# Performance work log

Hardware: AMD Instinct MI355X
Metric: run time of the kernel (lower is better)

Reference implementation:

```python
import jax, jax.numpy as jnp
import numpy as np

B, S, E, H = 4, 2048, 512, 8
DH = E // H
EPS = 1e-5

def _ln(x, g, b):
    m = jnp.mean(x, axis=-1, keepdims=True)
    v = jnp.var(x, axis=-1, keepdims=True)
    return (x - m) * jax.lax.rsqrt(v + EPS) * g + b

def setup_inputs() -> dict:
    key = jax.random.key(0)
    ks = jax.random.split(key, 8)
    sc = 0.02
    return {
        "x": jax.random.normal(ks[0], (B, S, E), dtype=jnp.float32),
        "ln1_g": jnp.ones((E,), jnp.float32),
        "ln1_b": jnp.zeros((E,), jnp.float32),
        "in_proj_w": sc * jax.random.normal(ks[1], (3 * E, E), jnp.float32),
        "in_proj_b": jnp.zeros((3 * E,), jnp.float32),
        "out_w": sc * jax.random.normal(ks[2], (E, E), jnp.float32),
        "out_b": jnp.zeros((E,), jnp.float32),
        "ln2_g": jnp.ones((E,), jnp.float32),
        "ln2_b": jnp.zeros((E,), jnp.float32),
        "fc1_w": sc * jax.random.normal(ks[3], (E, E), jnp.float32),
        "fc1_b": jnp.zeros((E,), jnp.float32),
        "fc2_w": sc * jax.random.normal(ks[4], (E, E), jnp.float32),
        "fc2_b": jnp.zeros((E,), jnp.float32),
    }

def reference(x, ln1_g, ln1_b, in_proj_w, in_proj_b, out_w, out_b,
              ln2_g, ln2_b, fc1_w, fc1_b, fc2_w, fc2_b):
    # pre-LN
    z = _ln(x, ln1_g, ln1_b)
    # qkv projection (torch MHA packed in_proj: [3E, E])
    qkv = z @ in_proj_w.T + in_proj_b          # [B,S,3E]
    q, k, v = jnp.split(qkv, 3, axis=-1)
    q = q.reshape(B, S, H, DH)
    k = k.reshape(B, S, H, DH)
    v = v.reshape(B, S, H, DH)
    scores = jnp.einsum("bqhd,bkhd->bhqk", q, k) / np.sqrt(DH).astype(np.float32)
    causal = jnp.triu(jnp.ones((S, S), dtype=bool), k=1)  # True = masked
    neg = jnp.finfo(scores.dtype).min
    scores = jnp.where(causal, neg, scores)
    attn = jax.nn.softmax(scores, axis=-1)      # [B,H,S,S]
    ctx = jnp.einsum("bhqk,bkhd->bqhd", attn, v).reshape(B, S, E)
    attn_out = ctx @ out_w.T + out_b
    # torch MHA with need_weights=True averages over heads by default
    attn_weights = jnp.mean(attn, axis=1)       # [B,S,S]
    z2 = x + attn_out
    y = _ln(z2, ln2_g, ln2_b)
    y = jax.nn.leaky_relu(y @ fc1_w.T + fc1_b, negative_slope=0.01)
    y = y @ fc2_w.T + fc2_b
    y = y + z2
    return (y, attn_weights)
```

## Files before the change

kernel.cpp:

```cpp
#include <hip/hip_runtime.h>

typedef short bf16x8 __attribute__((ext_vector_type(8)));
typedef float f32x4 __attribute__((ext_vector_type(4)));
typedef unsigned short u16x8 __attribute__((ext_vector_type(8)));

#define NB 4
#define SQ 2048
#define EM 512
#define NH 8
#define DHD 64
#define QSCALE 0.1803368801111731f

__device__ __forceinline__ unsigned short f2bf(float x) {
  unsigned u = __float_as_uint(x);
  u += 0x7FFFu + ((u >> 16) & 1u);
  return (unsigned short)(u >> 16);
}

__device__ __forceinline__ int sw8(int row, int col8) { return col8 ^ ((row & 7) << 3); }

__global__ __launch_bounds__(256) void f2bf_kernel(const float* __restrict__ in,
                                                   unsigned short* __restrict__ out, int n) {
  int i = (blockIdx.x * 256 + threadIdx.x) * 8;
  if (i >= n) return;
  f32x4 a = *(const f32x4*)(in + i);
  f32x4 b = *(const f32x4*)(in + i + 4);
  u16x8 o;
#pragma unroll
  for (int j = 0; j < 4; ++j) { o[j] = f2bf(a[j]); o[j + 4] = f2bf(b[j]); }
  *(u16x8*)(out + i) = o;
}

__global__ __launch_bounds__(256) void ln_kernel(const float* __restrict__ x,
                                                 const float* __restrict__ g,
                                                 const float* __restrict__ bb,
                                                 unsigned short* __restrict__ out) {
  int tid = threadIdx.x;
  int row = blockIdx.x * 4 + (tid >> 6);
  int lane = tid & 63;
  size_t base = (size_t)row * EM + lane * 8;
  f32x4 v0 = *(const f32x4*)(x + base);
  f32x4 v1 = *(const f32x4*)(x + base + 4);
  float s = 0.f, q = 0.f;
#pragma unroll
  for (int j = 0; j < 4; ++j) { s += v0[j] + v1[j]; q += v0[j] * v0[j] + v1[j] * v1[j]; }
#pragma unroll
  for (int m = 1; m < 64; m <<= 1) { s += __shfl_xor(s, m); q += __shfl_xor(q, m); }
  float mean = s * (1.f / EM);
  float var = q * (1.f / EM) - mean * mean;
  float rs = rsqrtf(var + 1e-5f);
  f32x4 g0 = *(const f32x4*)(g + lane * 8), g1 = *(const f32x4*)(g + lane * 8 + 4);
  f32x4 b0 = *(const f32x4*)(bb + lane * 8), b1 = *(const f32x4*)(bb + lane * 8 + 4);
  u16x8 o;
#pragma unroll
  for (int j = 0; j < 4; ++j) {
    o[j] = f2bf((v0[j] - mean) * rs * g0[j] + b0[j]);
    o[j + 4] = f2bf((v1[j] - mean) * rs * g1[j] + b1[j]);
  }
  *(u16x8*)(out + base) = o;
}

template <bool LEAKY, bool RESID, bool OUTF32, bool QKV>
__global__ __launch_bounds__(256) void gemm64(
    const unsigned short* __restrict__ A, const unsigned short* __restrict__ Bm,
    const float* __restrict__ bias, const float* __restrict__ resid,
    float* __restrict__ outf, unsigned short* __restrict__ outh,
    unsigned short* __restrict__ qo, unsigned short* __restrict__ ko,
    unsigned short* __restrict__ vo, int M, int N, int K) {
  __shared__ unsigned short As[64][64];
  __shared__ unsigned short Bs[64][64];
  int m0 = blockIdx.x * 64, n0 = blockIdx.y * 64;
  int t = threadIdx.x;
  int ar = t >> 2, ac = (t & 3) * 16;
  int wv = t >> 6, ln = t & 63, lg = ln >> 4, lr = ln & 15;
  f32x4 acc[4];
#pragma unroll
  for (int c = 0; c < 4; ++c)
#pragma unroll
    for (int r = 0; r < 4; ++r) acc[c][r] = 0.f;

  const unsigned short* ag = A + (size_t)(m0 + ar) * K + ac;
  const unsigned short* bg = Bm + (size_t)(n0 + ar) * K + ac;
  for (int k0 = 0; k0 < K; k0 += 64) {
    u16x8 a0 = *(const u16x8*)(ag + k0);
    u16x8 a1 = *(const u16x8*)(ag + k0 + 8);
    u16x8 b0 = *(const u16x8*)(bg + k0);
    u16x8 b1 = *(const u16x8*)(bg + k0 + 8);
    *(u16x8*)&As[ar][sw8(ar, ac)] = a0;
    *(u16x8*)&As[ar][sw8(ar, ac + 8)] = a1;
    *(u16x8*)&Bs[ar][sw8(ar, ac)] = b0;
    *(u16x8*)&Bs[ar][sw8(ar, ac + 8)] = b1;
    __syncthreads();
#pragma unroll
    for (int kk = 0; kk < 64; kk += 32) {
      int arw = wv * 16 + lr;
      bf16x8 af = *(const bf16x8*)&As[arw][sw8(arw, kk + lg * 8)];
#pragma unroll
      for (int c = 0; c < 4; ++c) {
        int brw = c * 16 + lr;
        bf16x8 bf = *(const bf16x8*)&Bs[brw][sw8(brw, kk + lg * 8)];
        acc[c] = __builtin_amdgcn_mfma_f32_16x16x32_bf16(af, bf, acc[c], 0, 0, 0);
      }
    }
    __syncthreads();
  }
#pragma unroll
  for (int c = 0; c < 4; ++c) {
    int C_ = n0 + c * 16 + lr;
    float bv = bias[C_];
#pragma unroll
    for (int r = 0; r < 4; ++r) {
      int R_ = m0 + wv * 16 + lg * 4 + r;
      float v = acc[c][r] + bv;
      if (LEAKY) v = v > 0.f ? v : 0.01f * v;
      if (RESID) v += resid[(size_t)R_ * N + C_];
      if (QKV) {
        int which = C_ >> 9, f = C_ & 511, h = f >> 6, d = f & 63;
        int b_ = R_ >> 11, s_ = R_ & 2047;
        if (which == 0) {
          qo[(((size_t)b_ * NH + h) * SQ + s_) * DHD + d] = f2bf(v * QSCALE);
        } else if (which == 1) {
          ko[(((size_t)b_ * NH + h) * SQ + s_) * DHD + d] = f2bf(v);
        } else {
          vo[(((size_t)b_ * NH + h) * DHD + d) * SQ + s_] = f2bf(v);
        }
      } else if (OUTF32) {
        outf[(size_t)R_ * N + C_] = v;
      } else {
        outh[(size_t)R_ * N + C_] = f2bf(v);
      }
    }
  }
}

__global__ __launch_bounds__(256) void flash_kernel(
    const unsigned short* __restrict__ Q, const unsigned short* __restrict__ Kb,
    const unsigned short* __restrict__ Vt, unsigned short* __restrict__ ctx,
    float* __restrict__ mstat, float* __restrict__ lstat) {
  __shared__ unsigned short Ks[2][64][64];
  __shared__ unsigned short Vs[2][64][64];
  __shared__ unsigned short Ps[4][16][64];
  int h = blockIdx.y, b = blockIdx.z;
  int t = threadIdx.x, wv = t >> 6, ln = t & 63, lg = ln >> 4, lr = ln & 15;
  int ar = t >> 2, ac = (t & 3) * 16;
  size_t headoff = ((size_t)b * NH + h) * SQ;
  const unsigned short* kgb = Kb + (headoff + ar) * DHD + ac;
  const unsigned short* vgb = Vt + (((size_t)b * NH + h) * DHD + ar) * SQ + ac;

  bf16x8 vones;
#pragma unroll
  for (int j = 0; j < 8; ++j) vones[j] = (lr == 0) ? (short)0x3F80 : (short)0;

  for (int half = 0; half < 2; ++half) {
    int qt = half ? blockIdx.x : (31 - blockIdx.x);
    int qb = qt * 64;
    const unsigned short* qrow = Q + (headoff + qb + wv * 16 + lr) * DHD;
    bf16x8 aq0 = *(const bf16x8*)(qrow + lg * 8);
    bf16x8 aq1 = *(const bf16x8*)(qrow + 32 + lg * 8);

    f32x4 cacc[4], lacc;
#pragma unroll
    for (int nd = 0; nd < 4; ++nd)
#pragma unroll
      for (int r = 0; r < 4; ++r) cacc[nd][r] = 0.f;
#pragma unroll
    for (int r = 0; r < 4; ++r) lacc[r] = 0.f;
    float mrun[4];
#pragma unroll
    for (int r = 0; r < 4; ++r) mrun[r] = -__builtin_inff();

    int nkt = qt + 1;
    __syncthreads();
    u16x8 kr0 = *(const u16x8*)(kgb);
    u16x8 kr1 = *(const u16x8*)(kgb + 8);
    u16x8 vr0 = *(const u16x8*)(vgb);
    u16x8 vr1 = *(const u16x8*)(vgb + 8);
    *(u16x8*)&Ks[0][ar][sw8(ar, ac)] = kr0;
    *(u16x8*)&Ks[0][ar][sw8(ar, ac + 8)] = kr1;
    *(u16x8*)&Vs[0][ar][sw8(ar, ac)] = vr0;
    *(u16x8*)&Vs[0][ar][sw8(ar, ac + 8)] = vr1;
    if (nkt > 1) {
      kr0 = *(const u16x8*)(kgb + (size_t)64 * DHD);
      kr1 = *(const u16x8*)(kgb + (size_t)64 * DHD + 8);
      vr0 = *(const u16x8*)(vgb + 64);
      vr1 = *(const u16x8*)(vgb + 64 + 8);
    }

    for (int kt = 0; kt < nkt; ++kt) {
      int cur = kt & 1;
      __syncthreads();
      if (kt + 1 < nkt) {
        int nb = cur ^ 1;
        *(u16x8*)&Ks[nb][ar][sw8(ar, ac)] = kr0;
        *(u16x8*)&Ks[nb][ar][sw8(ar, ac + 8)] = kr1;
        *(u16x8*)&Vs[nb][ar][sw8(ar, ac)] = vr0;
        *(u16x8*)&Vs[nb][ar][sw8(ar, ac + 8)] = vr1;
        if (kt + 2 < nkt) {
          size_t ko2 = (size_t)(kt + 2) * 64;
          kr0 = *(const u16x8*)(kgb + ko2 * DHD);
          kr1 = *(const u16x8*)(kgb + ko2 * DHD + 8);
          vr0 = *(const u16x8*)(vgb + ko2);
          vr1 = *(const u16x8*)(vgb + ko2 + 8);
        }
      }

      float sv[4][4];
      __builtin_amdgcn_s_setprio(1);
#pragma unroll
      for (int nt = 0; nt < 4; ++nt) {
        f32x4 sf;
#pragma unroll
        for (int r = 0; r < 4; ++r) sf[r] = 0.f;
        int brw = nt * 16 + lr;
        bf16x8 bk0 = *(const bf16x8*)&Ks[cur][brw][sw8(brw, lg * 8)];
        bf16x8 bk1 = *(const bf16x8*)&Ks[cur][brw][sw8(brw, 32 + lg * 8)];
        sf = __builtin_amdgcn_mfma_f32_16x16x32_bf16(aq0, bk0, sf, 0, 0, 0);
        sf = __builtin_amdgcn_mfma_f32_16x16x32_bf16(aq1, bk1, sf, 0, 0, 0);
#pragma unroll
        for (int r = 0; r < 4; ++r) sv[nt][r] = sf[r];
      }
      __builtin_amdgcn_s_setprio(0);
      if (kt == nkt - 1) {
        int kbase = kt * 64;
#pragma unroll
        for (int nt = 0; nt < 4; ++nt) {
          int kcol = kbase + nt * 16 + lr;
#pragma unroll
          for (int r = 0; r < 4; ++r) {
            int qr = qb + wv * 16 + lg * 4 + r;
            if (kcol > qr) sv[nt][r] = -__builtin_inff();
          }
        }
      }

      float tmax[4], needmax = 0.f;
#pragma unroll
      for (int r = 0; r < 4; ++r) {
        float tm = fmaxf(fmaxf(sv[0][r], sv[1][r]), fmaxf(sv[2][r], sv[3][r]));
#pragma unroll
        for (int m = 1; m < 16; m <<= 1) tm = fmaxf(tm, __shfl_xor(tm, m));
        tmax[r] = tm;
        needmax = fmaxf(needmax, tm - mrun[r]);
      }
      if (__any(needmax > 8.f)) {
#pragma unroll
        for (int r = 0; r < 4; ++r) {
          float mn = fmaxf(mrun[r], tmax[r]);
          float sc = exp2f(mrun[r] - mn);
          mrun[r] = mn;
          lacc[r] *= sc;
#pragma unroll
          for (int nd = 0; nd < 4; ++nd) cacc[nd][r] *= sc;
        }
      }
#pragma unroll
      for (int r = 0; r < 4; ++r) {
        int prow = lg * 4 + r;
#pragma unroll
        for (int nt = 0; nt < 4; ++nt) {
          float p = exp2f(sv[nt][r] - mrun[r]);
          Ps[wv][prow][sw8(prow, nt * 16 + lr)] = f2bf(p);
        }
      }

      bf16x8 pf0 = *(const bf16x8*)&Ps[wv][lr][sw8(lr, lg * 8)];
      bf16x8 pf1 = *(const bf16x8*)&Ps[wv][lr][sw8(lr, 32 + lg * 8)];
      __builtin_amdgcn_s_setprio(1);
      lacc = __builtin_amdgcn_mfma_f32_16x16x32_bf16(pf0, vones, lacc, 0, 0, 0);
      lacc = __builtin_amdgcn_mfma_f32_16x16x32_bf16(pf1, vones, lacc, 0, 0, 0);
#pragma unroll
      for (int nd = 0; nd < 4; ++nd) {
        int vrw = nd * 16 + lr;
        bf16x8 vf0 = *(const bf16x8*)&Vs[cur][vrw][sw8(vrw, lg * 8)];
        bf16x8 vf1 = *(const bf16x8*)&Vs[cur][vrw][sw8(vrw, 32 + lg * 8)];
        cacc[nd] = __builtin_amdgcn_mfma_f32_16x16x32_bf16(pf0, vf0, cacc[nd], 0, 0, 0);
        cacc[nd] = __builtin_amdgcn_mfma_f32_16x16x32_bf16(pf1, vf1, cacc[nd], 0, 0, 0);
      }
      __builtin_amdgcn_s_setprio(0);
    }

    float inv[4];
#pragma unroll
    for (int r = 0; r < 4; ++r) inv[r] = 1.f / __shfl(lacc[r], ln & 48);
#pragma unroll
    for (int nd = 0; nd < 4; ++nd)
#pragma unroll
      for (int r = 0; r < 4; ++r) {
        size_t dst = ((size_t)b * SQ + qb + wv * 16 + lg * 4 + r) * EM + h * DHD + nd * 16 + lr;
        ctx[dst] = f2bf(cacc[nd][r] * inv[r]);
      }
    if (lr == 0) {
#pragma unroll
      for (int r = 0; r < 4; ++r) {
        int row = qb + wv * 16 + lg * 4 + r;
        mstat[headoff + row] = mrun[r];
        lstat[headoff + row] = 0.125f * inv[r];
      }
    }
  }
}

__global__ __launch_bounds__(256) void attnw_kernel(
    const unsigned short* __restrict__ Q, const unsigned short* __restrict__ Kb,
    const float* __restrict__ mstat, const float* __restrict__ lstat,
    float* __restrict__ aw) {
  int kt = blockIdx.x, qt = blockIdx.y, b = blockIdx.z;
  int qb = qt * 64, kb = kt * 64;
  int t = threadIdx.x;
  float* tile = aw + ((size_t)b * SQ + qb) * SQ + kb;
  if (kt > qt) {
    int row = t >> 2, c = (t & 3) * 16;
    f32x4 z;
#pragma unroll
    for (int j = 0; j < 4; ++j) z[j] = 0.f;
    float* p = tile + (size_t)row * SQ + c;
    *(f32x4*)p = z; *(f32x4*)(p + 4) = z; *(f32x4*)(p + 8) = z; *(f32x4*)(p + 12) = z;
    return;
  }
  __shared__ unsigned short Ks[2][64][64];
  int wv = t >> 6, ln = t & 63, lg = ln >> 4, lr = ln & 15;
  int sr = t >> 2, sc8 = (t & 3) * 16;
  bool diag = (kt == qt);
  size_t khstride = (size_t)SQ * DHD;
  const unsigned short* kg = Kb + (((size_t)b * NH) * SQ + kb + sr) * DHD + sc8;
  const unsigned short* qg = Q + (((size_t)b * NH) * SQ + qb + wv * 16 + lr) * DHD + lg * 8;
  size_t mbase = (size_t)b * NH * SQ + qb + wv * 16 + lg * 4;

  u16x8 ka = *(const u16x8*)kg;
  u16x8 kx = *(const u16x8*)(kg + 8);
  *(u16x8*)&Ks[0][sr][sw8(sr, sc8)] = ka;
  *(u16x8*)&Ks[0][sr][sw8(sr, sc8 + 8)] = kx;
  ka = *(const u16x8*)(kg + khstride);
  kx = *(const u16x8*)(kg + khstride + 8);

  bf16x8 aqc0 = *(const bf16x8*)qg;
  bf16x8 aqc1 = *(const bf16x8*)(qg + 32);
  bf16x8 aqn0 = *(const bf16x8*)(qg + khstride);
  bf16x8 aqn1 = *(const bf16x8*)(qg + khstride + 32);
  float mmc[4], lic[4], mmn[4], lin[4];
#pragma unroll
  for (int r = 0; r < 4; ++r) {
    mmc[r] = mstat[mbase + r];
    lic[r] = lstat[mbase + r];
    mmn[r] = mstat[mbase + SQ + r];
    lin[r] = lstat[mbase + SQ + r];
  }

  f32x4 facc[4];
#pragma unroll
  for (int nt = 0; nt < 4; ++nt)
#pragma unroll
    for (int r = 0; r < 4; ++r) facc[nt][r] = 0.f;

  for (int h = 0; h < NH; ++h) {
    int cur = h & 1;
    __syncthreads();
    if (h + 1 < NH) {
      *(u16x8*)&Ks[cur ^ 1][sr][sw8(sr, sc8)] = ka;
      *(u16x8*)&Ks[cur ^ 1][sr][sw8(sr, sc8 + 8)] = kx;
      if (h + 2 < NH) {
        ka = *(const u16x8*)(kg + (size_t)(h + 2) * khstride);
        kx = *(const u16x8*)(kg + (size_t)(h + 2) * khstride + 8);
      }
    }

#pragma unroll
    for (int nt = 0; nt < 4; ++nt) {
      f32x4 sf;
#pragma unroll
      for (int r = 0; r < 4; ++r) sf[r] = 0.f;
      int brw = nt * 16 + lr;
      bf16x8 bk0 = *(const bf16x8*)&Ks[cur][brw][sw8(brw, lg * 8)];
      bf16x8 bk1 = *(const bf16x8*)&Ks[cur][brw][sw8(brw, 32 + lg * 8)];
      sf = __builtin_amdgcn_mfma_f32_16x16x32_bf16(aqc0, bk0, sf, 0, 0, 0);
      sf = __builtin_amdgcn_mfma_f32_16x16x32_bf16(aqc1, bk1, sf, 0, 0, 0);
#pragma unroll
      for (int r = 0; r < 4; ++r) facc[nt][r] += exp2f(sf[r] - mmc[r]) * lic[r];
    }

    aqc0 = aqn0; aqc1 = aqn1;
#pragma unroll
    for (int r = 0; r < 4; ++r) { mmc[r] = mmn[r]; lic[r] = lin[r]; }
    if (h + 2 < NH) {
      aqn0 = *(const bf16x8*)(qg + (size_t)(h + 2) * khstride);
      aqn1 = *(const bf16x8*)(qg + (size_t)(h + 2) * khstride + 32);
#pragma unroll
      for (int r = 0; r < 4; ++r) {
        mmn[r] = mstat[mbase + (size_t)(h + 2) * SQ + r];
        lin[r] = lstat[mbase + (size_t)(h + 2) * SQ + r];
      }
    }
  }

#pragma unroll
  for (int nt = 0; nt < 4; ++nt) {
    int kc = kb + nt * 16 + lr;
#pragma unroll
    for (int r = 0; r < 4; ++r) {
      int qr = qb + wv * 16 + lg * 4 + r;
      float v = (diag && kc > qr) ? 0.f : facc[nt][r];
      tile[(size_t)(wv * 16 + lg * 4 + r) * SQ + nt * 16 + lr] = v;
    }
  }
}

extern "C" void kernel_launch(void* const* d_in, const int* in_sizes, int n_in,
                              void* d_out, int out_size, void* d_ws, size_t ws_size,
                              hipStream_t stream) {
  (void)in_sizes; (void)n_in; (void)out_size; (void)ws_size;
  const float* x = (const float*)d_in[0];
  const float* ln1g = (const float*)d_in[1];
  const float* ln1b = (const float*)d_in[2];
  const float* wqkv = (const float*)d_in[3];
  const float* bqkv = (const float*)d_in[4];
  const float* wout = (const float*)d_in[5];
  const float* bout = (const float*)d_in[6];
  const float* ln2g = (const float*)d_in[7];
  const float* ln2b = (const float*)d_in[8];
  const float* wfc1 = (const float*)d_in[9];
  const float* bfc1 = (const float*)d_in[10];
  const float* wfc2 = (const float*)d_in[11];
  const float* bfc2 = (const float*)d_in[12];

  char* ws = (char*)d_ws;
  unsigned short* zctx = (unsigned short*)(ws);
  unsigned short* qb_ = (unsigned short*)(ws + 8388608);
  unsigned short* kb_ = (unsigned short*)(ws + 16777216);
  unsigned short* vb_ = (unsigned short*)(ws + 25165824);
  float* z2 = (float*)(ws + 33554432);
  float* mstat = (float*)(ws + 50331648);
  float* lstat = (float*)(ws + 50593792);
  unsigned short* wqkv_h = (unsigned short*)(ws + 50855936);
  unsigned short* wout_h = (unsigned short*)(ws + 52428800);
  unsigned short* wfc1_h = (unsigned short*)(ws + 52953088);
  unsigned short* wfc2_h = (unsigned short*)(ws + 53477376);
  unsigned short* y1 = qb_;
  unsigned short* h1 = kb_;

  float* outy = (float*)d_out;
  float* outw = outy + (size_t)NB * SQ * EM;

  f2bf_kernel<<<384, 256, 0, stream>>>(wqkv, wqkv_h, 786432);
  f2bf_kernel<<<128, 256, 0, stream>>>(wout, wout_h, 262144);
  f2bf_kernel<<<128, 256, 0, stream>>>(wfc1, wfc1_h, 262144);
  f2bf_kernel<<<128, 256, 0, stream>>>(wfc2, wfc2_h, 262144);

  ln_kernel<<<2048, 256, 0, stream>>>(x, ln1g, ln1b, zctx);
  gemm64<false, false, false, true><<<dim3(128, 24), 256, 0, stream>>>(
      zctx, wqkv_h, bqkv, nullptr, nullptr, nullptr, qb_, kb_, vb_, 8192, 1536, 512);
  flash_kernel<<<dim3(16, 8, 4), 256, 0, stream>>>(qb_, kb_, vb_, zctx, mstat, lstat);
  attnw_kernel<<<dim3(32, 32, 4), 256, 0, stream>>>(qb_, kb_, mstat, lstat, outw);
  gemm64<false, true, true, false><<<dim3(128, 8), 256, 0, stream>>>(
      zctx, wout_h, bout, x, z2, nullptr, nullptr, nullptr, nullptr, 8192, 512, 512);
  ln_kernel<<<2048, 256, 0, stream>>>(z2, ln2g, ln2b, y1);
  gemm64<true, false, false, false><<<dim3(128, 8), 256, 0, stream>>>(
      y1, wfc1_h, bfc1, nullptr, nullptr, h1, nullptr, nullptr, nullptr, 8192, 512, 512);
  gemm64<false, true, true, false><<<dim3(128, 8), 256, 0, stream>>>(
      h1, wfc2_h, bfc2, z2, outy, nullptr, nullptr, nullptr, nullptr, 8192, 512, 512);
}
```

Baseline: 204.0 us.

## Use direct global-to-LDS loads with double buffering and lazy row-max reduction

```diff
diff --git a/kernel.cpp b/kernel.cpp
--- a/kernel.cpp
+++ b/kernel.cpp
@@ -18,6 +18,12 @@
 }
 
 __device__ __forceinline__ int sw8(int row, int col8) { return col8 ^ ((row & 7) << 3); }
+
+__device__ __forceinline__ void glds16(const void* g, void* l) {
+  __builtin_amdgcn_global_load_lds(
+      (const __attribute__((address_space(1))) void*)g,
+      (__attribute__((address_space(3))) void*)l, 16, 0, 0);
+}
 
 __global__ __launch_bounds__(256) void f2bf_kernel(const float* __restrict__ in,
                                                    unsigned short* __restrict__ out, int n) {
@@ -67,42 +73,52 @@
     float* __restrict__ outf, unsigned short* __restrict__ outh,
     unsigned short* __restrict__ qo, unsigned short* __restrict__ ko,
     unsigned short* __restrict__ vo, int M, int N, int K) {
-  __shared__ unsigned short As[64][64];
-  __shared__ unsigned short Bs[64][64];
+  __shared__ unsigned short As[2][64][64];
+  __shared__ unsigned short Bs[2][64][64];
   int m0 = blockIdx.x * 64, n0 = blockIdx.y * 64;
   int t = threadIdx.x;
-  int ar = t >> 2, ac = (t & 3) * 16;
   int wv = t >> 6, ln = t & 63, lg = ln >> 4, lr = ln & 15;
+  int rsub = ln >> 3;
+  int csw = ((ln & 7) ^ rsub) * 8;
   f32x4 acc[4];
 #pragma unroll
   for (int c = 0; c < 4; ++c)
 #pragma unroll
     for (int r = 0; r < 4; ++r) acc[c][r] = 0.f;
 
-  const unsigned short* ag = A + (size_t)(m0 + ar) * K + ac;
-  const unsigned short* bg = Bm + (size_t)(n0 + ar) * K + ac;
-  for (int k0 = 0; k0 < K; k0 += 64) {
-    u16x8 a0 = *(const u16x8*)(ag + k0);
-    u16x8 a1 = *(const u16x8*)(ag + k0 + 8);
-    u16x8 b0 = *(const u16x8*)(bg + k0);
-    u16x8 b1 = *(const u16x8*)(bg + k0 + 8);
-    *(u16x8*)&As[ar][sw8(ar, ac)] = a0;
-    *(u16x8*)&As[ar][sw8(ar, ac + 8)] = a1;
-    *(u16x8*)&Bs[ar][sw8(ar, ac)] = b0;
-    *(u16x8*)&Bs[ar][sw8(ar, ac + 8)] = b1;
+  const unsigned short* ag0 = A + (size_t)(m0 + wv * 16 + rsub) * K + csw;
+  const unsigned short* ag1 = A + (size_t)(m0 + wv * 16 + 8 + rsub) * K + csw;
+  const unsigned short* bg0 = Bm + (size_t)(n0 + wv * 16 + rsub) * K + csw;
+  const unsigned short* bg1 = Bm + (size_t)(n0 + wv * 16 + 8 + rsub) * K + csw;
+
+  glds16(ag0, &As[0][wv * 16][0]);
+  glds16(ag1, &As[0][wv * 16 + 8][0]);
+  glds16(bg0, &Bs[0][wv * 16][0]);
+  glds16(bg1, &Bs[0][wv * 16 + 8][0]);
+
+  int nk = K >> 6;
+  for (int ki = 0; ki < nk; ++ki) {
+    int cur = ki & 1;
     __syncthreads();
+    if (ki + 1 < nk) {
+      int nb = cur ^ 1;
+      int ko_ = (ki + 1) * 64;
+      glds16(ag0 + ko_, &As[nb][wv * 16][0]);
+      glds16(ag1 + ko_, &As[nb][wv * 16 + 8][0]);
+      glds16(bg0 + ko_, &Bs[nb][wv * 16][0]);
+      glds16(bg1 + ko_, &Bs[nb][wv * 16 + 8][0]);
+    }
 #pragma unroll
     for (int kk = 0; kk < 64; kk += 32) {
       int arw = wv * 16 + lr;
-      bf16x8 af = *(const bf16x8*)&As[arw][sw8(arw, kk + lg * 8)];
+      bf16x8 af = *(const bf16x8*)&As[cur][arw][sw8(arw, kk + lg * 8)];
 #pragma unroll
       for (int c = 0; c < 4; ++c) {
         int brw = c * 16 + lr;
-        bf16x8 bf = *(const bf16x8*)&Bs[brw][sw8(brw, kk + lg * 8)];
+        bf16x8 bf = *(const bf16x8*)&Bs[cur][brw][sw8(brw, kk + lg * 8)];
         acc[c] = __builtin_amdgcn_mfma_f32_16x16x32_bf16(af, bf, acc[c], 0, 0, 0);
       }
     }
-    __syncthreads();
   }
 #pragma unroll
   for (int c = 0; c < 4; ++c) {
@@ -142,10 +158,13 @@
   __shared__ unsigned short Ps[4][16][64];
   int h = blockIdx.y, b = blockIdx.z;
   int t = threadIdx.x, wv = t >> 6, ln = t & 63, lg = ln >> 4, lr = ln & 15;
-  int ar = t >> 2, ac = (t & 3) * 16;
+  int rsub = ln >> 3;
+  int csw = ((ln & 7) ^ rsub) * 8;
   size_t headoff = ((size_t)b * NH + h) * SQ;
-  const unsigned short* kgb = Kb + (headoff + ar) * DHD + ac;
-  const unsigned short* vgb = Vt + (((size_t)b * NH + h) * DHD + ar) * SQ + ac;
+  const unsigned short* kg0 = Kb + (headoff + wv * 16 + rsub) * DHD + csw;
+  const unsigned short* kg1 = Kb + (headoff + wv * 16 + 8 + rsub) * DHD + csw;
+  const unsigned short* vg0 = Vt + (((size_t)b * NH + h) * DHD + wv * 16 + rsub) * SQ + csw;
+  const unsigned short* vg1 = Vt + (((size_t)b * NH + h) * DHD + wv * 16 + 8 + rsub) * SQ + csw;
 
   bf16x8 vones;
 #pragma unroll
@@ -171,37 +190,21 @@
 
     int nkt = qt + 1;
     __syncthreads();
-    u16x8 kr0 = *(const u16x8*)(kgb);
-    u16x8 kr1 = *(const u16x8*)(kgb + 8);
-    u16x8 vr0 = *(const u16x8*)(vgb);
-    u16x8 vr1 = *(const u16x8*)(vgb + 8);
-    *(u16x8*)&Ks[0][ar][sw8(ar, ac)] = kr0;
-    *(u16x8*)&Ks[0][ar][sw8(ar, ac + 8)] = kr1;
-    *(u16x8*)&Vs[0][ar][sw8(ar, ac)] = vr0;
-    *(u16x8*)&Vs[0][ar][sw8(ar, ac + 8)] = vr1;
-    if (nkt > 1) {
-      kr0 = *(const u16x8*)(kgb + (size_t)64 * DHD);
-      kr1 = *(const u16x8*)(kgb + (size_t)64 * DHD + 8);
-      vr0 = *(const u16x8*)(vgb + 64);
-      vr1 = *(const u16x8*)(vgb + 64 + 8);
-    }
+    glds16(kg0, &Ks[0][wv * 16][0]);
+    glds16(kg1, &Ks[0][wv * 16 + 8][0]);
+    glds16(vg0, &Vs[0][wv * 16][0]);
+    glds16(vg1, &Vs[0][wv * 16 + 8][0]);
 
     for (int kt = 0; kt < nkt; ++kt) {
       int cur = kt & 1;
       __syncthreads();
       if (kt + 1 < nkt) {
         int nb = cur ^ 1;
-        *(u16x8*)&Ks[nb][ar][sw8(ar, ac)] = kr0;
-        *(u16x8*)&Ks[nb][ar][sw8(ar, ac + 8)] = kr1;
-        *(u16x8*)&Vs[nb][ar][sw8(ar, ac)] = vr0;
-        *(u16x8*)&Vs[nb][ar][sw8(ar, ac + 8)] = vr1;
-        if (kt + 2 < nkt) {
-          size_t ko2 = (size_t)(kt + 2) * 64;
-          kr0 = *(const u16x8*)(kgb + ko2 * DHD);
-          kr1 = *(const u16x8*)(kgb + ko2 * DHD + 8);
-          vr0 = *(const u16x8*)(vgb + ko2);
-          vr1 = *(const u16x8*)(vgb + ko2 + 8);
-        }
+        size_t ko_ = (size_t)(kt + 1) * 64;
+        glds16(kg0 + ko_ * DHD, &Ks[nb][wv * 16][0]);
+        glds16(kg1 + ko_ * DHD, &Ks[nb][wv * 16 + 8][0]);
+        glds16(vg0 + ko_, &Vs[nb][wv * 16][0]);
+        glds16(vg1 + ko_, &Vs[nb][wv * 16 + 8][0]);
       }
 
       float sv[4][4];
@@ -233,19 +236,20 @@
         }
       }
 
-      float tmax[4], needmax = 0.f;
+      float lmax[4];
+      bool need = false;
 #pragma unroll
       for (int r = 0; r < 4; ++r) {
-        float tm = fmaxf(fmaxf(sv[0][r], sv[1][r]), fmaxf(sv[2][r], sv[3][r]));
-#pragma unroll
-        for (int m = 1; m < 16; m <<= 1) tm = fmaxf(tm, __shfl_xor(tm, m));
-        tmax[r] = tm;
-        needmax = fmaxf(needmax, tm - mrun[r]);
-      }
-      if (__any(needmax > 8.f)) {
+        lmax[r] = fmaxf(fmaxf(sv[0][r], sv[1][r]), fmaxf(sv[2][r], sv[3][r]));
+        need |= (lmax[r] > mrun[r] + 8.f);
+      }
+      if (__any(need)) {
 #pragma unroll
         for (int r = 0; r < 4; ++r) {
-          float mn = fmaxf(mrun[r], tmax[r]);
+          float tm = lmax[r];
+#pragma unroll
+          for (int m = 1; m < 16; m <<= 1) tm = fmaxf(tm, __shfl_xor(tm, m));
+          float mn = fmaxf(mrun[r], tm);
           float sc = exp2f(mrun[r] - mn);
           mrun[r] = mn;
           lacc[r] *= sc;
@@ -319,19 +323,17 @@
   }
   __shared__ unsigned short Ks[2][64][64];
   int wv = t >> 6, ln = t & 63, lg = ln >> 4, lr = ln & 15;
-  int sr = t >> 2, sc8 = (t & 3) * 16;
+  int rsub = ln >> 3;
+  int csw = ((ln & 7) ^ rsub) * 8;
   bool diag = (kt == qt);
   size_t khstride = (size_t)SQ * DHD;
-  const unsigned short* kg = Kb + (((size_t)b * NH) * SQ + kb + sr) * DHD + sc8;
+  const unsigned short* kg0 = Kb + (((size_t)b * NH) * SQ + kb + wv * 16 + rsub) * DHD + csw;
+  const unsigned short* kg1 = Kb + (((size_t)b * NH) * SQ + kb + wv * 16 + 8 + rsub) * DHD + csw;
   const unsigned short* qg = Q + (((size_t)b * NH) * SQ + qb + wv * 16 + lr) * DHD + lg * 8;
   size_t mbase = (size_t)b * NH * SQ + qb + wv * 16 + lg * 4;
 
-  u16x8 ka = *(const u16x8*)kg;
-  u16x8 kx = *(const u16x8*)(kg + 8);
-  *(u16x8*)&Ks[0][sr][sw8(sr, sc8)] = ka;
-  *(u16x8*)&Ks[0][sr][sw8(sr, sc8 + 8)] = kx;
-  ka = *(const u16x8*)(kg + khstride);
-  kx = *(const u16x8*)(kg + khstride + 8);
+  glds16(kg0, &Ks[0][wv * 16][0]);
+  glds16(kg1, &Ks[0][wv * 16 + 8][0]);
 
   bf16x8 aqc0 = *(const bf16x8*)qg;
   bf16x8 aqc1 = *(const bf16x8*)(qg + 32);
@@ -356,12 +358,8 @@
     int cur = h & 1;
     __syncthreads();
     if (h + 1 < NH) {
-      *(u16x8*)&Ks[cur ^ 1][sr][sw8(sr, sc8)] = ka;
-      *(u16x8*)&Ks[cur ^ 1][sr][sw8(sr, sc8 + 8)] = kx;
-      if (h + 2 < NH) {
-        ka = *(const u16x8*)(kg + (size_t)(h + 2) * khstride);
-        kx = *(const u16x8*)(kg + (size_t)(h + 2) * khstride + 8);
-      }
+      glds16(kg0 + (size_t)(h + 1) * khstride, &Ks[cur ^ 1][wv * 16][0]);
+      glds16(kg1 + (size_t)(h + 1) * khstride, &Ks[cur ^ 1][wv * 16 + 8][0]);
     }
 
 #pragma unroll
```

Result: faster. 198.8 us (-2.5%).
